# Optimization experiments

Hardware: AMD Instinct MI355X
Metric: run time of the kernel (lower is better)

The kernel has to match this reference:

```python
import jax, jax.numpy as jnp
import numpy as np

N = 100000
H = 4      # heads
C = 32     # hidden per head (out_channels)
DIN = 9
NEG_SLOPE = 0.2  # PyG GATConv default


def gat_layer(x, src, dst, W, a_src, a_dst, b):
    # x: [N, F] -> h: [N, H, C]
    h = (x @ W).reshape(-1, H, C)
    s = (h * a_src).sum(-1)  # [N, H]
    d = (h * a_dst).sum(-1)  # [N, H]
    alpha = jax.nn.leaky_relu(s[src] + d[dst], negative_slope=NEG_SLOPE)  # [E, H]
    # segment softmax over incoming edges of each dst node
    amax = jax.ops.segment_max(alpha, dst, num_segments=N)
    e = jnp.exp(alpha - amax[dst])
    denom = jax.ops.segment_sum(e, dst, num_segments=N)
    w = e / denom[dst]                                   # [E, H]
    msg = h[src] * w[:, :, None]                          # [E, H, C]
    out = jax.ops.segment_sum(msg, dst, num_segments=N)  # [N, H, C]
    return out.mean(axis=1) + b                           # concat=False -> mean heads


def setup_inputs():
    key = jax.random.key(0)
    ks = jax.random.split(key, 16)
    E = 1600000
    EL = 500000
    sc = lambda *sh: 1.0 / np.sqrt(sh[0])
    inp = {
        "x": jax.random.normal(ks[0], (N, DIN), jnp.float32),
        "edge_index": jax.random.randint(ks[1], (2, E), 0, N, jnp.int32),
        "edge_label_index": jax.random.randint(ks[2], (2, EL), 0, N, jnp.int32),
        "W1": jax.random.normal(ks[3], (DIN, H * C), jnp.float32) * sc(DIN),
        "a_src1": jax.random.normal(ks[4], (H, C), jnp.float32) * sc(C),
        "a_dst1": jax.random.normal(ks[5], (H, C), jnp.float32) * sc(C),
        "b1": jnp.zeros((C,), jnp.float32),
        "W2": jax.random.normal(ks[6], (C, H * C), jnp.float32) * sc(C),
        "a_src2": jax.random.normal(ks[7], (H, C), jnp.float32) * sc(C),
        "a_dst2": jax.random.normal(ks[8], (H, C), jnp.float32) * sc(C),
        "b2": jnp.zeros((C,), jnp.float32),
        "Wn": jax.random.normal(ks[9], (C, 2), jnp.float32) * sc(C),
        "bn": jnp.zeros((2,), jnp.float32),
        "We1": jax.random.normal(ks[10], (2 * C, 64), jnp.float32) * sc(2 * C),
        "be1": jnp.zeros((64,), jnp.float32),
        "We2": jax.random.normal(ks[11], (64, 1), jnp.float32) * sc(64),
        "be2": jnp.zeros((1,), jnp.float32),
    }
    return inp


def reference(x, edge_index, edge_label_index, W1, a_src1, a_dst1, b1, W2, a_src2, a_dst2, b2, Wn, bn, We1, be1, We2, be2):
    # add self loops (PyG GATConv default)
    loop = jnp.arange(N, dtype=edge_index.dtype)
    src = jnp.concatenate([edge_index[0], loop])
    dst = jnp.concatenate([edge_index[1], loop])

    h = jax.nn.relu(gat_layer(x, src, dst, W1, a_src1, a_dst1, b1))
    h = jax.nn.relu(gat_layer(h, src, dst, W2, a_src2, a_dst2, b2))
    # dropout is identity in eval mode
    node_logits = h @ Wn + bn  # [N, 2]

    ei = jnp.concatenate([h[edge_label_index[0]], h[edge_label_index[1]]], axis=1)  # [EL, 2C]
    edge_logits = jax.nn.relu(ei @ We1 + be1) @ We2 + be2  # [EL, 1]
    return node_logits, edge_logits
```

## Files before the change

### kernel.cpp

```cpp
#include <hip/hip_runtime.h>
#include <hip/hip_fp16.h>


#define NPART 8

using half8 = __attribute__((ext_vector_type(8))) _Float16;
using floatx4 = __attribute__((ext_vector_type(4))) float;

__global__ void hist_part_kernel(const int* __restrict__ dst, int E, int* __restrict__ cnt,
                                 int partSize) {
  int p = blockIdx.x & (NPART - 1);
  int sblk = blockIdx.x >> 3;
  int nsb = gridDim.x >> 3;
  int lo = p * partSize, hi = lo + partSize;
  int stride = nsb * blockDim.x;
  for (int i = sblk * blockDim.x + threadIdx.x; i < E; i += stride) {
    int dv = dst[i];
    if (dv >= lo && dv < hi) atomicAdd(&cnt[dv], 1);
  }
}

__global__ void scatter_part_kernel(const int* __restrict__ src, const int* __restrict__ dst,
                                    int E, int* __restrict__ cursor, int* __restrict__ esrc,
                                    int partSize) {
  int p = blockIdx.x & (NPART - 1);
  int sblk = blockIdx.x >> 3;
  int nsb = gridDim.x >> 3;
  int lo = p * partSize, hi = lo + partSize;
  int stride = nsb * blockDim.x;
  for (int i = sblk * blockDim.x + threadIdx.x; i < E; i += stride) {
    int dv = dst[i];
    if (dv >= lo && dv < hi) {
      int pos = atomicAdd(&cursor[dv], 1);
      esrc[pos] = src[i];
    }
  }
}

__global__ __launch_bounds__(256) void scan_part_kernel(const int* __restrict__ cnt, int n,
                                                        int* __restrict__ part) {
  __shared__ int ws[4];
  int b = blockIdx.x;
  int tid = threadIdx.x;
  int base = b * 1024 + tid * 4;
  int s = 0;
#pragma unroll
  for (int q = 0; q < 4; ++q) {
    int i = base + q;
    s += (i < n) ? cnt[i] : 0;
  }
#pragma unroll
  for (int m = 1; m < 64; m <<= 1) s += __shfl_xor(s, m);
  if ((tid & 63) == 0) ws[tid >> 6] = s;
  __syncthreads();
  if (tid == 0) part[b] = ws[0] + ws[1] + ws[2] + ws[3];
}

__global__ __launch_bounds__(256) void scan_mid_kernel(int* part, int nb, int* offs_total,
                                                       int addN) {
  __shared__ int buf[512];
  int tid = threadIdx.x;
  for (int i = tid; i < nb; i += 256) buf[i] = part[i];
  __syncthreads();
  if (tid == 0) {
    int t = 0;
    for (int i = 0; i < nb; ++i) { int v = buf[i]; buf[i] = t; t += v; }
    *offs_total = t + addN;
  }
  __syncthreads();
  for (int i = tid; i < nb; i += 256) part[i] = buf[i];
}

__global__ __launch_bounds__(256) void scan_fix_kernel(const int* __restrict__ cnt, int n,
                                                       const int* __restrict__ part,
                                                       int* __restrict__ offs,
                                                       int* __restrict__ cursor,
                                                       int* __restrict__ esrc) {
  __shared__ int ws[4];
  int b = blockIdx.x;
  int tid = threadIdx.x;
  int lane = tid & 63;
  int w = tid >> 6;
  int base = b * 1024 + tid * 4;
  int v[4];
#pragma unroll
  for (int q = 0; q < 4; ++q) {
    int i = base + q;
    v[q] = (i < n) ? cnt[i] : 0;
  }
  int tsum = v[0] + v[1] + v[2] + v[3];
  int x = tsum;
#pragma unroll
  for (int m = 1; m < 64; m <<= 1) {
    int up = __shfl_up(x, m);
    if (lane >= m) x += up;
  }
  if (lane == 63) ws[w] = x;
  __syncthreads();
  int woff = 0;
#pragma unroll
  for (int k = 0; k < 4; ++k) woff += (k < w) ? ws[k] : 0;
  int runc = part[b] + woff + (x - tsum);
#pragma unroll
  for (int q = 0; q < 4; ++q) {
    int i = base + q;
    if (i < n) {
      offs[i] = runc + i;
      cursor[i] = runc + i;
      esrc[runc + i + v[q]] = i;
    }
    runc += v[q];
  }
}

template <bool L1>
__global__ __launch_bounds__(256) void transform_mfma_kernel(
    const float* __restrict__ xf, const __half* __restrict__ xh,
    const float* __restrict__ W, int Keff,
    const float* __restrict__ a_src, const float* __restrict__ a_dst,
    __half* __restrict__ h, float* __restrict__ s, float* __restrict__ d, int N) {
  int lane = threadIdx.x & 63;
  int quad = lane >> 4;
  int col = lane & 15;

  half8 af[8];
#pragma unroll
  for (int ct = 0; ct < 8; ++ct) {
#pragma unroll
    for (int j = 0; j < 8; ++j) {
      int k = quad * 8 + j;
      af[ct][j] = (k < Keff) ? (_Float16)W[k * 128 + ct * 16 + col] : (_Float16)0.f;
    }
  }

  int ntile = (N + 15) >> 4;
  int wstep = gridDim.x * 4;
  for (int tile = blockIdx.x * 4 + (threadIdx.x >> 6); tile < ntile; tile += wstep) {
    int node = tile * 16 + col;
    int nclamp = min(node, N - 1);

    half8 bfr;
    if (L1) {
      const float* xr = xf + (size_t)nclamp * 9;
#pragma unroll
      for (int j = 0; j < 8; ++j) {
        int k = quad * 8 + j;
        bfr[j] = (k < 9) ? (_Float16)xr[k] : (_Float16)0.f;
      }
    } else {
      bfr = *(const half8*)(xh + (size_t)nclamp * 32 + quad * 8);
    }

    floatx4 acc[8];
#pragma unroll
    for (int ct = 0; ct < 8; ++ct) acc[ct] = (floatx4){0.f, 0.f, 0.f, 0.f};
#pragma unroll
    for (int ct = 0; ct < 8; ++ct)
      acc[ct] = __builtin_amdgcn_mfma_f32_16x16x32_f16(af[ct], bfr, acc[ct], 0, 0, 0);

    float sp[4] = {0.f, 0.f, 0.f, 0.f}, dp[4] = {0.f, 0.f, 0.f, 0.f};
    bool wr = (node < N);
#pragma unroll
    for (int ct = 0; ct < 8; ++ct) {
      int f0 = ct * 16 + quad * 4;
      if (wr) {
        __half2 p0 = __floats2half2_rn(acc[ct][0], acc[ct][1]);
        __half2 p1 = __floats2half2_rn(acc[ct][2], acc[ct][3]);
        __half2* hp = (__half2*)(h + (size_t)node * 128 + f0);
        hp[0] = p0;
        hp[1] = p1;
      }
      int hh = ct >> 1;
      const float4 av = *(const float4*)(a_src + f0);
      const float4 dv = *(const float4*)(a_dst + f0);
      sp[hh] += acc[ct][0] * av.x + acc[ct][1] * av.y + acc[ct][2] * av.z + acc[ct][3] * av.w;
      dp[hh] += acc[ct][0] * dv.x + acc[ct][1] * dv.y + acc[ct][2] * dv.z + acc[ct][3] * dv.w;
    }
#pragma unroll
    for (int hh = 0; hh < 4; ++hh) {
      sp[hh] += __shfl_xor(sp[hh], 16);
      sp[hh] += __shfl_xor(sp[hh], 32);
      dp[hh] += __shfl_xor(dp[hh], 16);
      dp[hh] += __shfl_xor(dp[hh], 32);
    }
    if (quad == 0 && wr) {
      *(float4*)(s + node * 4) = make_float4(sp[0], sp[1], sp[2], sp[3]);
      *(float4*)(d + node * 4) = make_float4(dp[0], dp[1], dp[2], dp[3]);
    }
  }
}

__global__ void aggregate_kernel(const __half* __restrict__ h, const float* __restrict__ s,
                                 const float* __restrict__ d, const int* __restrict__ offs,
                                 const int* __restrict__ esrc, const float* __restrict__ bias,
                                 float* __restrict__ out, __half* __restrict__ out16,
                                 const float* __restrict__ Wn, const float* __restrict__ bn,
                                 float* __restrict__ out_node, int N) {
  int wid = blockIdx.x * (blockDim.x >> 6) + (threadIdx.x >> 6);
  if (wid >= N) return;
  int lane = threadIdx.x & 63;
  int g = lane >> 4;
  int k = lane & 15;
  int head = k >> 2;
  float dsel = d[wid * 4 + head];
  int beg = offs[wid], end = offs[wid + 1];
  int cnt = end - beg;
  int M = (cnt + 3) >> 2;
  int i0 = beg + g;
  int last = end - 1;
  const half8* hrow = (const half8*)h;

  float acc[8] = {0.f, 0.f, 0.f, 0.f, 0.f, 0.f, 0.f, 0.f};
  float den = 0.f;

  int src0 = esrc[min(i0, last)];
  int src1 = esrc[min(i0 + 4, last)];
  float sv0 = s[src0 * 4 + head];
  half8 hv0 = hrow[(size_t)src0 * 16 + k];
  float sv1 = s[src1 * 4 + head];
  half8 hv1 = hrow[(size_t)src1 * 16 + k];
  int src2 = esrc[min(i0 + 8, last)];

  for (int t = 0; t < M; ++t) {
    float sv2 = s[src2 * 4 + head];
    half8 hv2 = hrow[(size_t)src2 * 16 + k];
    int src3 = esrc[min(i0 + 4 * (t + 3), last)];
    float a = sv0 + dsel;
    a = fmaxf(a, 0.2f * a);
    float e = __expf(a);
    e = (i0 + 4 * t < end) ? e : 0.f;
    den += e;
    const __half2* hp = (const __half2*)&hv0;
#pragma unroll
    for (int q = 0; q < 4; ++q) {
      float2 f = __half22float2(hp[q]);
      acc[2 * q] = fmaf(e, f.x, acc[2 * q]);
      acc[2 * q + 1] = fmaf(e, f.y, acc[2 * q + 1]);
    }
    sv0 = sv1; hv0 = hv1; sv1 = sv2; hv1 = hv2; src2 = src3;
  }

  den += __shfl_xor(den, 16);
  den += __shfl_xor(den, 32);
#pragma unroll
  for (int q = 0; q < 8; ++q) {
    acc[q] += __shfl_xor(acc[q], 16);
    acc[q] += __shfl_xor(acc[q], 32);
  }
  float inv = 1.f / den;
#pragma unroll
  for (int q = 0; q < 8; ++q) {
    acc[q] *= inv;
    acc[q] += __shfl_xor(acc[q], 4);
    acc[q] += __shfl_xor(acc[q], 8);
  }
  if (lane < 4) {
#pragma unroll
    for (int q = 0; q < 8; ++q)
      acc[q] = fmaxf(acc[q] * 0.25f + bias[8 * k + q], 0.f);
    if (out) {
      float4 o0 = make_float4(acc[0], acc[1], acc[2], acc[3]);
      float4 o1 = make_float4(acc[4], acc[5], acc[6], acc[7]);
      ((float4*)out)[(size_t)wid * 8 + 2 * k] = o0;
      ((float4*)out)[(size_t)wid * 8 + 2 * k + 1] = o1;
    }
    if (out16) {
      half8 hv;
#pragma unroll
      for (int q = 0; q < 8; ++q) hv[q] = (_Float16)acc[q];
      ((half8*)out16)[(size_t)wid * 4 + k] = hv;
    }
    if (Wn) {
      float p0 = 0.f, p1 = 0.f;
#pragma unroll
      for (int q = 0; q < 8; ++q) {
        int c = 8 * k + q;
        p0 = fmaf(acc[q], Wn[c * 2], p0);
        p1 = fmaf(acc[q], Wn[c * 2 + 1], p1);
      }
      p0 += __shfl_xor(p0, 1); p1 += __shfl_xor(p1, 1);
      p0 += __shfl_xor(p0, 2); p1 += __shfl_xor(p1, 2);
      if (k == 0) {
        out_node[wid * 2] = p0 + bn[0];
        out_node[wid * 2 + 1] = p1 + bn[1];
      }
    }
  }
}

__global__ __launch_bounds__(256) void edge_head_mfma_kernel(
    const __half* __restrict__ h2, const int* __restrict__ eli, int EL,
    const float* __restrict__ We1, const float* __restrict__ be1,
    const float* __restrict__ We2, const float* __restrict__ be2, float* __restrict__ out) {
  int lane = threadIdx.x & 63;
  int quad = lane >> 4;
  int col = lane & 15;

  half8 bf[2][4];
#pragma unroll
  for (int ks = 0; ks < 2; ++ks)
#pragma unroll
    for (int nt = 0; nt < 4; ++nt)
#pragma unroll
      for (int i = 0; i < 8; ++i)
        bf[ks][nt][i] = (_Float16)We1[(ks * 32 + quad * 8 + i) * 64 + nt * 16 + col];

  float b1v[4], w2v[4];
#pragma unroll
  for (int nt = 0; nt < 4; ++nt) {
    b1v[nt] = be1[nt * 16 + col];
    w2v[nt] = We2[nt * 16 + col];
  }
  float be2v = be2[0];

  int ngroups = (EL + 15) >> 4;
  int wstep = gridDim.x * 4;
  for (int group = blockIdx.x * 4 + (threadIdx.x >> 6); group < ngroups; group += wstep) {
    int e = min(group * 16 + col, EL - 1);
    int a = eli[e];
    int b = eli[EL + e];
    half8 af0 = *(const half8*)(h2 + (size_t)a * 32 + quad * 8);
    half8 af1 = *(const half8*)(h2 + (size_t)b * 32 + quad * 8);

    floatx4 acc[4];
#pragma unroll
    for (int nt = 0; nt < 4; ++nt) acc[nt] = (floatx4){0.f, 0.f, 0.f, 0.f};
#pragma unroll
    for (int nt = 0; nt < 4; ++nt)
      acc[nt] = __builtin_amdgcn_mfma_f32_16x16x32_f16(af0, bf[0][nt], acc[nt], 0, 0, 0);
#pragma unroll
    for (int nt = 0; nt < 4; ++nt)
      acc[nt] = __builtin_amdgcn_mfma_f32_16x16x32_f16(af1, bf[1][nt], acc[nt], 0, 0, 0);

#pragma unroll
    for (int reg = 0; reg < 4; ++reg) {
      float p = 0.f;
#pragma unroll
      for (int nt = 0; nt < 4; ++nt) {
        float z = acc[nt][reg] + b1v[nt];
        z = fmaxf(z, 0.f);
        p = fmaf(z, w2v[nt], p);
      }
      p += __shfl_xor(p, 1);
      p += __shfl_xor(p, 2);
      p += __shfl_xor(p, 4);
      p += __shfl_xor(p, 8);
      if (col == 0) {
        int eo = group * 16 + quad * 4 + reg;
        if (eo < EL) out[eo] = p + be2v;
      }
    }
  }
}

extern "C" void kernel_launch(void* const* d_in, const int* in_sizes, int n_in,
                              void* d_out, int out_size, void* d_ws, size_t ws_size,
                              hipStream_t stream) {
  const float* x = (const float*)d_in[0];
  const int* ei = (const int*)d_in[1];
  const int* eli = (const int*)d_in[2];
  const float* W1 = (const float*)d_in[3];
  const float* a_src1 = (const float*)d_in[4];
  const float* a_dst1 = (const float*)d_in[5];
  const float* b1 = (const float*)d_in[6];
  const float* W2 = (const float*)d_in[7];
  const float* a_src2 = (const float*)d_in[8];
  const float* a_dst2 = (const float*)d_in[9];
  const float* b2 = (const float*)d_in[10];
  const float* Wn = (const float*)d_in[11];
  const float* bn = (const float*)d_in[12];
  const float* We1 = (const float*)d_in[13];
  const float* be1 = (const float*)d_in[14];
  const float* We2 = (const float*)d_in[15];
  const float* be2 = (const float*)d_in[16];

  const int N = in_sizes[0] / 9;
  const int E = in_sizes[1] / 2;
  const int EL = in_sizes[2] / 2;

  float* wsf = (float*)d_ws;
  __half* h_half = (__half*)wsf;
  float* sbuf = wsf + (size_t)N * 64;
  float* dbuf = sbuf + (size_t)N * 4;
  __half* h1h = (__half*)(wsf + (size_t)N * 72);
  __half* h2h = (__half*)(wsf + (size_t)N * 88);
  int* offs = (int*)(wsf + (size_t)N * 104);
  int* cursor = offs + (N + 1);
  int* esrc = cursor + N;
  int* part = esrc + (E + N);

  float* out_node = (float*)d_out;
  float* out_edge = out_node + (size_t)N * 2;

  const int B = 256;
  const int wavesPerBlock = B / 64;
  int gridNwave = (N + wavesPerBlock - 1) / wavesPerBlock;
  int nb = (N + 1023) / 1024;
  int partSize = (N + NPART - 1) / NPART;
  int gridPart = NPART * 192;

  hipMemsetAsync(cursor, 0, (size_t)N * sizeof(int), stream);
  hist_part_kernel<<<gridPart, B, 0, stream>>>(ei + E, E, cursor, partSize);
  scan_part_kernel<<<nb, B, 0, stream>>>(cursor, N, part);
  scan_mid_kernel<<<1, B, 0, stream>>>(part, nb, offs + N, N);
  scan_fix_kernel<<<nb, B, 0, stream>>>(cursor, N, part, offs, cursor, esrc);
  scatter_part_kernel<<<gridPart, B, 0, stream>>>(ei, ei + E, E, cursor, esrc, partSize);

  transform_mfma_kernel<true><<<512, B, 0, stream>>>(x, nullptr, W1, 9, a_src1, a_dst1,
                                                     h_half, sbuf, dbuf, N);
  aggregate_kernel<<<gridNwave, B, 0, stream>>>(h_half, sbuf, dbuf, offs, esrc, b1,
                                                nullptr, h1h, nullptr, nullptr, nullptr, N);

  transform_mfma_kernel<false><<<512, B, 0, stream>>>(nullptr, h1h, W2, 32, a_src2, a_dst2,
                                                      h_half, sbuf, dbuf, N);
  aggregate_kernel<<<gridNwave, B, 0, stream>>>(h_half, sbuf, dbuf, offs, esrc, b2,
                                                nullptr, h2h, Wn, bn, out_node, N);

  edge_head_mfma_kernel<<<1024, B, 0, stream>>>(h2h, eli, EL, We1, be1, We2, be2, out_edge);
}
```

Measured before the change: 460.0 us.

## Fuse CSR scatter with layer-1 transform; restructure aggregate prefetch pipeline

Merges the edge scatter kernel and the first-layer MFMA transform into one launch, with blocks split by index into scatter and transform roles so the two independent stages run concurrently. The template is removed and the layer-2 transform becomes its own kernel. Separately, the aggregate loop is unrolled by two with two independent prefetch streams, which is meant to keep more gathers in flight. This costs extra registers and some code duplication, and a few excess loads past the end of each segment, though these are clamped.

```diff
diff --git a/kernel.cpp b/kernel.cpp
--- a/kernel.cpp
+++ b/kernel.cpp
@@ -17,23 +17,6 @@
   for (int i = sblk * blockDim.x + threadIdx.x; i < E; i += stride) {
     int dv = dst[i];
     if (dv >= lo && dv < hi) atomicAdd(&cnt[dv], 1);
-  }
-}
-
-__global__ void scatter_part_kernel(const int* __restrict__ src, const int* __restrict__ dst,
-                                    int E, int* __restrict__ cursor, int* __restrict__ esrc,
-                                    int partSize) {
-  int p = blockIdx.x & (NPART - 1);
-  int sblk = blockIdx.x >> 3;
-  int nsb = gridDim.x >> 3;
-  int lo = p * partSize, hi = lo + partSize;
-  int stride = nsb * blockDim.x;
-  for (int i = sblk * blockDim.x + threadIdx.x; i < E; i += stride) {
-    int dv = dst[i];
-    if (dv >= lo && dv < hi) {
-      int pos = atomicAdd(&cursor[dv], 1);
-      esrc[pos] = src[i];
-    }
   }
 }
 
@@ -113,51 +96,119 @@
   }
 }
 
-template <bool L1>
+__global__ __launch_bounds__(256) void scatter_transform_kernel(
+    const int* __restrict__ src, const int* __restrict__ dst, int E,
+    int* __restrict__ cursor, int* __restrict__ esrc, int partSize, int scatterBlocks,
+    const float* __restrict__ xf, const float* __restrict__ W,
+    const float* __restrict__ a_src, const float* __restrict__ a_dst,
+    __half* __restrict__ h, float* __restrict__ s, float* __restrict__ d, int N) {
+  if (blockIdx.x < scatterBlocks) {
+    int p = blockIdx.x & (NPART - 1);
+    int sblk = blockIdx.x >> 3;
+    int nsb = scatterBlocks >> 3;
+    int lo = p * partSize, hi = lo + partSize;
+    int stride = nsb * blockDim.x;
+    for (int i = sblk * blockDim.x + threadIdx.x; i < E; i += stride) {
+      int dv = dst[i];
+      if (dv >= lo && dv < hi) {
+        int pos = atomicAdd(&cursor[dv], 1);
+        esrc[pos] = src[i];
+      }
+    }
+    return;
+  }
+  int lane = threadIdx.x & 63;
+  int quad = lane >> 4;
+  int col = lane & 15;
+  half8 af[8];
+#pragma unroll
+  for (int ct = 0; ct < 8; ++ct) {
+#pragma unroll
+    for (int j = 0; j < 8; ++j) {
+      int k = quad * 8 + j;
+      af[ct][j] = (k < 9) ? (_Float16)W[k * 128 + ct * 16 + col] : (_Float16)0.f;
+    }
+  }
+  int nTB = gridDim.x - scatterBlocks;
+  int ntile = (N + 15) >> 4;
+  int wstep = nTB * 4;
+  for (int tile = (blockIdx.x - scatterBlocks) * 4 + (threadIdx.x >> 6); tile < ntile;
+       tile += wstep) {
+    int node = tile * 16 + col;
+    int nclamp = min(node, N - 1);
+    half8 bfr;
+    const float* xr = xf + (size_t)nclamp * 9;
+#pragma unroll
+    for (int j = 0; j < 8; ++j) {
+      int k = quad * 8 + j;
+      bfr[j] = (k < 9) ? (_Float16)xr[k] : (_Float16)0.f;
+    }
+    floatx4 acc[8];
+#pragma unroll
+    for (int ct = 0; ct < 8; ++ct) acc[ct] = (floatx4){0.f, 0.f, 0.f, 0.f};
+#pragma unroll
+    for (int ct = 0; ct < 8; ++ct)
+      acc[ct] = __builtin_amdgcn_mfma_f32_16x16x32_f16(af[ct], bfr, acc[ct], 0, 0, 0);
+    float sp[4] = {0.f, 0.f, 0.f, 0.f}, dp[4] = {0.f, 0.f, 0.f, 0.f};
+    bool wr = (node < N);
+#pragma unroll
+    for (int ct = 0; ct < 8; ++ct) {
+      int f0 = ct * 16 + quad * 4;
+      if (wr) {
+        __half2 p0 = __floats2half2_rn(acc[ct][0], acc[ct][1]);
+        __half2 p1 = __floats2half2_rn(acc[ct][2], acc[ct][3]);
+        __half2* hp = (__half2*)(h + (size_t)node * 128 + f0);
+        hp[0] = p0;
+        hp[1] = p1;
+      }
+      int hh = ct >> 1;
+      const float4 av = *(const float4*)(a_src + f0);
+      const float4 dv = *(const float4*)(a_dst + f0);
+      sp[hh] += acc[ct][0] * av.x + acc[ct][1] * av.y + acc[ct][2] * av.z + acc[ct][3] * av.w;
+      dp[hh] += acc[ct][0] * dv.x + acc[ct][1] * dv.y + acc[ct][2] * dv.z + acc[ct][3] * dv.w;
+    }
+#pragma unroll
+    for (int hh = 0; hh < 4; ++hh) {
+      sp[hh] += __shfl_xor(sp[hh], 16);
+      sp[hh] += __shfl_xor(sp[hh], 32);
+      dp[hh] += __shfl_xor(dp[hh], 16);
+      dp[hh] += __shfl_xor(dp[hh], 32);
+    }
+    if (quad == 0 && wr) {
+      *(float4*)(s + node * 4) = make_float4(sp[0], sp[1], sp[2], sp[3]);
+      *(float4*)(d + node * 4) = make_float4(dp[0], dp[1], dp[2], dp[3]);
+    }
+  }
+}
+
 __global__ __launch_bounds__(256) void transform_mfma_kernel(
-    const float* __restrict__ xf, const __half* __restrict__ xh,
-    const float* __restrict__ W, int Keff,
+    const __half* __restrict__ xh, const float* __restrict__ W,
     const float* __restrict__ a_src, const float* __restrict__ a_dst,
     __half* __restrict__ h, float* __restrict__ s, float* __restrict__ d, int N) {
   int lane = threadIdx.x & 63;
   int quad = lane >> 4;
   int col = lane & 15;
-
   half8 af[8];
 #pragma unroll
   for (int ct = 0; ct < 8; ++ct) {
 #pragma unroll
     for (int j = 0; j < 8; ++j) {
       int k = quad * 8 + j;
-      af[ct][j] = (k < Keff) ? (_Float16)W[k * 128 + ct * 16 + col] : (_Float16)0.f;
-    }
-  }
-
+      af[ct][j] = (_Float16)W[k * 128 + ct * 16 + col];
+    }
+  }
   int ntile = (N + 15) >> 4;
   int wstep = gridDim.x * 4;
   for (int tile = blockIdx.x * 4 + (threadIdx.x >> 6); tile < ntile; tile += wstep) {
     int node = tile * 16 + col;
     int nclamp = min(node, N - 1);
-
-    half8 bfr;
-    if (L1) {
-      const float* xr = xf + (size_t)nclamp * 9;
-#pragma unroll
-      for (int j = 0; j < 8; ++j) {
-        int k = quad * 8 + j;
-        bfr[j] = (k < 9) ? (_Float16)xr[k] : (_Float16)0.f;
-      }
-    } else {
-      bfr = *(const half8*)(xh + (size_t)nclamp * 32 + quad * 8);
-    }
-
+    half8 bfr = *(const half8*)(xh + (size_t)nclamp * 32 + quad * 8);
     floatx4 acc[8];
 #pragma unroll
     for (int ct = 0; ct < 8; ++ct) acc[ct] = (floatx4){0.f, 0.f, 0.f, 0.f};
 #pragma unroll
     for (int ct = 0; ct < 8; ++ct)
       acc[ct] = __builtin_amdgcn_mfma_f32_16x16x32_f16(af[ct], bfr, acc[ct], 0, 0, 0);
-
     float sp[4] = {0.f, 0.f, 0.f, 0.f}, dp[4] = {0.f, 0.f, 0.f, 0.f};
     bool wr = (node < N);
 #pragma unroll
@@ -213,31 +264,52 @@
   float acc[8] = {0.f, 0.f, 0.f, 0.f, 0.f, 0.f, 0.f, 0.f};
   float den = 0.f;
 
-  int src0 = esrc[min(i0, last)];
-  int src1 = esrc[min(i0 + 4, last)];
-  float sv0 = s[src0 * 4 + head];
-  half8 hv0 = hrow[(size_t)src0 * 16 + k];
-  float sv1 = s[src1 * 4 + head];
-  half8 hv1 = hrow[(size_t)src1 * 16 + k];
-  int src2 = esrc[min(i0 + 8, last)];
-
-  for (int t = 0; t < M; ++t) {
-    float sv2 = s[src2 * 4 + head];
-    half8 hv2 = hrow[(size_t)src2 * 16 + k];
-    int src3 = esrc[min(i0 + 4 * (t + 3), last)];
-    float a = sv0 + dsel;
-    a = fmaxf(a, 0.2f * a);
-    float e = __expf(a);
-    e = (i0 + 4 * t < end) ? e : 0.f;
-    den += e;
-    const __half2* hp = (const __half2*)&hv0;
-#pragma unroll
-    for (int q = 0; q < 4; ++q) {
-      float2 f = __half22float2(hp[q]);
-      acc[2 * q] = fmaf(e, f.x, acc[2 * q]);
-      acc[2 * q + 1] = fmaf(e, f.y, acc[2 * q + 1]);
-    }
-    sv0 = sv1; hv0 = hv1; sv1 = sv2; hv1 = hv2; src2 = src3;
+  int srcA = esrc[min(i0, last)];
+  int srcB = esrc[min(i0 + 4, last)];
+  float sv0 = s[srcA * 4 + head];
+  half8 hv0 = hrow[(size_t)srcA * 16 + k];
+  float sv1 = s[srcB * 4 + head];
+  half8 hv1 = hrow[(size_t)srcB * 16 + k];
+  srcA = esrc[min(i0 + 8, last)];
+  srcB = esrc[min(i0 + 12, last)];
+
+  int Mp = (M + 1) >> 1;
+  for (int p = 0; p < Mp; ++p) {
+    int t = 2 * p;
+    {
+      float a = sv0 + dsel;
+      a = fmaxf(a, 0.2f * a);
+      float e = __expf(a);
+      e = (i0 + 4 * t < end) ? e : 0.f;
+      den += e;
+      const __half2* hp = (const __half2*)&hv0;
+#pragma unroll
+      for (int q = 0; q < 4; ++q) {
+        float2 f = __half22float2(hp[q]);
+        acc[2 * q] = fmaf(e, f.x, acc[2 * q]);
+        acc[2 * q + 1] = fmaf(e, f.y, acc[2 * q + 1]);
+      }
+    }
+    sv0 = s[srcA * 4 + head];
+    hv0 = hrow[(size_t)srcA * 16 + k];
+    srcA = esrc[min(i0 + 4 * (t + 4), last)];
+    {
+      float a = sv1 + dsel;
+      a = fmaxf(a, 0.2f * a);
+      float e = __expf(a);
+      e = (i0 + 4 * (t + 1) < end) ? e : 0.f;
+      den += e;
+      const __half2* hp = (const __half2*)&hv1;
+#pragma unroll
+      for (int q = 0; q < 4; ++q) {
+        float2 f = __half22float2(hp[q]);
+        acc[2 * q] = fmaf(e, f.x, acc[2 * q]);
+        acc[2 * q + 1] = fmaf(e, f.y, acc[2 * q + 1]);
+      }
+    }
+    sv1 = s[srcB * 4 + head];
+    hv1 = hrow[(size_t)srcB * 16 + k];
+    srcB = esrc[min(i0 + 4 * (t + 5), last)];
   }
 
   den += __shfl_xor(den, 16);
@@ -404,15 +476,15 @@
   scan_part_kernel<<<nb, B, 0, stream>>>(cursor, N, part);
   scan_mid_kernel<<<1, B, 0, stream>>>(part, nb, offs + N, N);
   scan_fix_kernel<<<nb, B, 0, stream>>>(cursor, N, part, offs, cursor, esrc);
-  scatter_part_kernel<<<gridPart, B, 0, stream>>>(ei, ei + E, E, cursor, esrc, partSize);
-
-  transform_mfma_kernel<true><<<512, B, 0, stream>>>(x, nullptr, W1, 9, a_src1, a_dst1,
-                                                     h_half, sbuf, dbuf, N);
+
+  scatter_transform_kernel<<<gridPart + 512, B, 0, stream>>>(
+      ei, ei + E, E, cursor, esrc, partSize, gridPart,
+      x, W1, a_src1, a_dst1, h_half, sbuf, dbuf, N);
   aggregate_kernel<<<gridNwave, B, 0, stream>>>(h_half, sbuf, dbuf, offs, esrc, b1,
                                                 nullptr, h1h, nullptr, nullptr, nullptr, N);
 
-  transform_mfma_kernel<false><<<512, B, 0, stream>>>(nullptr, h1h, W2, 32, a_src2, a_dst2,
-                                                      h_half, sbuf, dbuf, N);
+  transform_mfma_kernel<<<512, B, 0, stream>>>(h1h, W2, a_src2, a_dst2,
+                                               h_half, sbuf, dbuf, N);
   aggregate_kernel<<<gridNwave, B, 0, stream>>>(h_half, sbuf, dbuf, offs, esrc, b2,
                                                 nullptr, h2h, Wn, bn, out_node, N);
 
```

Measured after the change: 450.4 us. 1.02x faster.
